# Optimization experiments

Hardware: AMD Instinct MI355X
Metric: run time of the kernel (lower is better)

Reference implementation:

```python
import jax, jax.numpy as jnp
import numpy as np

D_MODEL = 512
HEAD = 64

def setup_inputs() -> dict:
    key = jax.random.key(0)
    ks = jax.random.split(key, 7)
    s_in = 1.0 / np.sqrt(D_MODEL)
    x = jax.random.normal(ks[0], (4, 4096, D_MODEL), dtype=jnp.float32)
    Wk = jax.random.uniform(ks[1], (D_MODEL, HEAD), jnp.float32, -s_in, s_in)
    bk = jax.random.uniform(ks[2], (HEAD,), jnp.float32, -s_in, s_in)
    Wq = jax.random.uniform(ks[3], (D_MODEL, HEAD), jnp.float32, -s_in, s_in)
    bq = jax.random.uniform(ks[4], (HEAD,), jnp.float32, -s_in, s_in)
    Wv = jax.random.uniform(ks[5], (D_MODEL, HEAD), jnp.float32, -s_in, s_in)
    bv = jax.random.uniform(ks[6], (HEAD,), jnp.float32, -s_in, s_in)
    return {"x": x, "Wk": Wk, "bk": bk, "Wq": Wq, "bq": bq, "Wv": Wv, "bv": bv}

def reference(x, Wk, bk, Wq, bq, Wv, bv):
    B, T, C = x.shape
    k = x @ Wk + bk            # [B,T,H]
    q = x @ Wq + bq            # [B,T,H]
    v = x @ Wv + bv            # [B,T,H]
    scale = C ** (-0.5)
    # NOTE: original computes k @ q^T (keys index rows), softmax over query axis
    w = jnp.einsum('bkh,bqh->bkq', k, q) * scale  # [B,T,T]
    w = jax.nn.softmax(w, axis=-1)
    out = jnp.einsum('bkq,bqh->bkh', w, v)        # [B,T,H]
    return out
```

## Files before the change

### kernel.cpp

```cpp
#include <hip/hip_runtime.h>


#define DM 512
#define HD 64
#define TSEQ 4096
#define KSCALE (1.4426950408889634f * 0.04419417382415922f)

typedef __attribute__((ext_vector_type(8))) __bf16 bf16x8;
typedef __attribute__((ext_vector_type(4))) __bf16 bf16x4;
typedef __attribute__((ext_vector_type(2))) __bf16 bf16x2;
typedef __attribute__((ext_vector_type(4))) float f32x4;
typedef __attribute__((ext_vector_type(16))) float f32x16;
typedef __attribute__((ext_vector_type(4))) unsigned int uint4v;

__device__ __forceinline__ float fast_exp2(float x) {
#if __has_builtin(__builtin_amdgcn_exp2f)
    return __builtin_amdgcn_exp2f(x);
#else
    return exp2f(x);
#endif
}

__device__ __forceinline__ bf16x8 ld_bf16x8(const unsigned short* p) {
    return __builtin_bit_cast(bf16x8, *(const uint4v*)p);
}
__device__ __forceinline__ f32x4 mfma16(bf16x8 a, bf16x8 b, f32x4 c) {
    return __builtin_amdgcn_mfma_f32_16x16x32_bf16(a, b, c, 0, 0, 0);
}
__device__ __forceinline__ f32x16 mfma32(bf16x8 a, bf16x8 b, f32x16 c) {
    return __builtin_amdgcn_mfma_f32_32x32x16_bf16(a, b, c, 0, 0, 0);
}

typedef const __attribute__((address_space(1))) unsigned int* gas_t;
typedef __attribute__((address_space(3))) unsigned int* las_t;
__device__ __forceinline__ void async_cp16(const void* g, void* l) {
    __builtin_amdgcn_global_load_lds((gas_t)(unsigned long long)g,
                                     (las_t)(unsigned int)(unsigned long long)l,
                                     16, 0, 0);
}

__global__ __launch_bounds__(256) void prep_wt(const float* __restrict__ Wk,
                                               const float* __restrict__ Wq,
                                               const float* __restrict__ Wv,
                                               unsigned short* __restrict__ WT) {
    int e = blockIdx.x * 256 + threadIdx.x;
    int m = e >> 15;
    int idx = e & 32767;
    int h = idx >> 9;
    int cc = idx & 511;
    const float* W = (m == 0) ? Wk : ((m == 1) ? Wq : Wv);
    float v = W[cc * HD + h];
    if (m == 0) v *= KSCALE;
    ((__bf16*)WT)[m * 32768 + h * DM + cc] = (__bf16)v;
}

__global__ __launch_bounds__(256, 4) void proj(const float* __restrict__ x,
                                               const unsigned short* __restrict__ WT,
                                               const float* __restrict__ bk,
                                               const float* __restrict__ bq,
                                               const float* __restrict__ bv,
                                               unsigned short* __restrict__ Kw,
                                               unsigned short* __restrict__ Qw,
                                               unsigned short* __restrict__ VTw) {
    __shared__ alignas(16) float xs[8192];
    const int tid = threadIdx.x;
    const int wv = tid >> 6, lane = tid & 63;
    const int c = lane & 15, quad = lane >> 4;
    const int bx = blockIdx.x;
    const int n0 = wv * 16;

#pragma unroll
    for (int r = 0; r < 8; ++r) {
        int cid = r * 256 + tid;
        int row = cid >> 7, pos = cid & 127;
        int g = (pos & ~7) | ((pos ^ row) & 7);
        async_cp16((const char*)x + (size_t)(bx * 16 + row) * 2048 + g * 16,
                   (char*)xs + r * 4096 + wv * 1024);
    }
    __builtin_amdgcn_s_waitcnt(0x0f70);
    __syncthreads();

    const unsigned short* wtb = WT + (n0 + c) * DM + quad * 8;
    f32x4 acc[3];
#pragma unroll
    for (int m = 0; m < 3; ++m) acc[m] = (f32x4){0.f, 0.f, 0.f, 0.f};

#pragma unroll
    for (int ks = 0; ks < 16; ++ks) {
        int p0 = ks * 8 + quad * 2;
        int sp0 = (p0 & ~7) | ((p0 ^ c) & 7);
        int sp1 = ((p0 + 1) & ~7) | (((p0 + 1) ^ c) & 7);
        f32x4 xa = *(const f32x4*)((const char*)xs + c * 2048 + sp0 * 16);
        f32x4 xb = *(const f32x4*)((const char*)xs + c * 2048 + sp1 * 16);
        bf16x8 af;
        af[0] = (__bf16)xa[0]; af[1] = (__bf16)xa[1]; af[2] = (__bf16)xa[2]; af[3] = (__bf16)xa[3];
        af[4] = (__bf16)xb[0]; af[5] = (__bf16)xb[1]; af[6] = (__bf16)xb[2]; af[7] = (__bf16)xb[3];
#pragma unroll
        for (int m = 0; m < 3; ++m) {
            bf16x8 bf = ld_bf16x8(wtb + m * 32768 + ks * 32);
            acc[m] = mfma16(af, bf, acc[m]);
        }
    }

    const int row0 = bx * 16 + quad * 4;
#pragma unroll
    for (int m = 0; m < 3; ++m) {
        const float* bp = (m == 0) ? bk : ((m == 1) ? bq : bv);
        float bias = bp[n0 + c];
        if (m == 0) bias *= KSCALE;
        if (m < 2) {
            __bf16* dst = (__bf16*)((m == 0) ? Kw : Qw);
#pragma unroll
            for (int r = 0; r < 4; ++r)
                dst[(row0 + r) * HD + n0 + c] = (__bf16)(acc[m][r] + bias);
        } else {
            bf16x4 pk;
#pragma unroll
            for (int r = 0; r < 4; ++r) pk[r] = (__bf16)(acc[m][r] + bias);
            int b = bx >> 8;
            int t16 = bx & 255;
            int pj = t16 >> 1;
            int jsub = (t16 & 1) * 16 + quad * 4;
            *(bf16x4*)(VTw + (((size_t)(b * 128 + pj)) * 64 + n0 + c) * 32 + jsub) = pk;
        }
    }
}

__global__ __launch_bounds__(512, 2) void attn(const unsigned short* __restrict__ Kw,
                                               const unsigned short* __restrict__ Qw,
                                               const unsigned short* __restrict__ VTw,
                                               float* __restrict__ Op,
                                               float* __restrict__ Lp) {
    __shared__ alignas(16) char smem[36864];

    const int tid = threadIdx.x;
    const int wv = tid >> 6, lane = tid & 63;
    const int l5 = lane >> 5, l31 = lane & 31;
    const int rg = wv >> 2, jc = wv & 3;
    const int bx = blockIdx.x;
    const int batch = bx >> 6, js = (bx >> 5) & 1, tile = bx & 31;
    const int rowbase = batch * TSEQ + tile * 128;

    bf16x8 kf[2][4];
#pragma unroll
    for (int it = 0; it < 2; ++it) {
        const unsigned short* kp = Kw + (size_t)(rowbase + rg * 64 + it * 32 + l31) * HD;
#pragma unroll
        for (int ks = 0; ks < 4; ++ks) kf[it][ks] = ld_bf16x8(kp + ks * 16 + l5 * 8);
    }

    const char* qg = (const char*)Qw
                   + ((size_t)(batch * TSEQ + js * 2048 + jc * 32 + l31)) * 128
                   + l5 * 16;
    const char* vg = (const char*)VTw
                   + ((size_t)(batch * 128 + js * 64 + jc)) * 4096
                   + l31 * 64 + l5 * 16;

    f32x16 o00, o01, o10, o11;
#pragma unroll
    for (int r = 0; r < 16; ++r) { o00[r] = 0.f; o01[r] = 0.f; o10[r] = 0.f; o11[r] = 0.f; }
    float lac0 = 0.f, lac1 = 0.f;

    bf16x8 qa[4], vf[2][2];
#pragma unroll
    for (int ks = 0; ks < 4; ++ks) qa[ks] = ld_bf16x8((const unsigned short*)(qg + ks * 32));
#pragma unroll
    for (int ht = 0; ht < 2; ++ht)
#pragma unroll
        for (int k2 = 0; k2 < 2; ++k2)
            vf[ht][k2] = ld_bf16x8((const unsigned short*)(vg + ht * 2048 + k2 * 32));

    for (int jt = 0; jt < 16; ++jt) {
        bf16x8 qn[4], vn[2][2];
        if (jt < 15) {
            const char* q1 = qg + (size_t)(jt + 1) * 16384;
            const char* v1 = vg + (size_t)(jt + 1) * 16384;
#pragma unroll
            for (int ks = 0; ks < 4; ++ks) qn[ks] = ld_bf16x8((const unsigned short*)(q1 + ks * 32));
#pragma unroll
            for (int ht = 0; ht < 2; ++ht)
#pragma unroll
                for (int k2 = 0; k2 < 2; ++k2)
                    vn[ht][k2] = ld_bf16x8((const unsigned short*)(v1 + ht * 2048 + k2 * 32));
        }

        f32x16 s0, s1;
#pragma unroll
        for (int r = 0; r < 16; ++r) { s0[r] = 0.f; s1[r] = 0.f; }
#pragma unroll
        for (int ks = 0; ks < 4; ++ks) {
            s0 = mfma32(qa[ks], kf[0][ks], s0);
            s1 = mfma32(qa[ks], kf[1][ks], s1);
        }

        unsigned int pk0[8], pk1[8];
#pragma unroll
        for (int m = 0; m < 8; ++m) {
            float a0 = fast_exp2(s0[2 * m]), a1 = fast_exp2(s0[2 * m + 1]);
            float b0 = fast_exp2(s1[2 * m]), b1 = fast_exp2(s1[2 * m + 1]);
            lac0 += a0 + a1;
            lac1 += b0 + b1;
            bf16x2 ta; ta[0] = (__bf16)a0; ta[1] = (__bf16)a1;
            bf16x2 tb; tb[0] = (__bf16)b0; tb[1] = (__bf16)b1;
            pk0[m] = __builtin_bit_cast(unsigned int, ta);
            pk1[m] = __builtin_bit_cast(unsigned int, tb);
        }

#pragma unroll
        for (int k2 = 0; k2 < 2; ++k2) {
            bf16x8 pb0, pb1;
            {
                unsigned int A0 = pk0[k2 * 4 + 0], A1 = pk0[k2 * 4 + 1];
                unsigned int B0 = pk0[k2 * 4 + 2], B1 = pk0[k2 * 4 + 3];
                unsigned int t0 = l5 ? A0 : B0, t1 = l5 ? A1 : B1;
                unsigned int r0 = (unsigned int)__shfl_xor((int)t0, 32, 64);
                unsigned int r1 = (unsigned int)__shfl_xor((int)t1, 32, 64);
                uint4v u;
                u[0] = l5 ? r0 : A0; u[1] = l5 ? r1 : A1;
                u[2] = l5 ? B0 : r0; u[3] = l5 ? B1 : r1;
                pb0 = __builtin_bit_cast(bf16x8, u);
            }
            {
                unsigned int A0 = pk1[k2 * 4 + 0], A1 = pk1[k2 * 4 + 1];
                unsigned int B0 = pk1[k2 * 4 + 2], B1 = pk1[k2 * 4 + 3];
                unsigned int t0 = l5 ? A0 : B0, t1 = l5 ? A1 : B1;
                unsigned int r0 = (unsigned int)__shfl_xor((int)t0, 32, 64);
                unsigned int r1 = (unsigned int)__shfl_xor((int)t1, 32, 64);
                uint4v u;
                u[0] = l5 ? r0 : A0; u[1] = l5 ? r1 : A1;
                u[2] = l5 ? B0 : r0; u[3] = l5 ? B1 : r1;
                pb1 = __builtin_bit_cast(bf16x8, u);
            }
            o00 = mfma32(vf[0][k2], pb0, o00);
            o01 = mfma32(vf[0][k2], pb1, o01);
            o10 = mfma32(vf[1][k2], pb0, o10);
            o11 = mfma32(vf[1][k2], pb1, o11);
        }

#pragma unroll
        for (int ks = 0; ks < 4; ++ks) qa[ks] = qn[ks];
#pragma unroll
        for (int ht = 0; ht < 2; ++ht)
#pragma unroll
            for (int k2 = 0; k2 < 2; ++k2) vf[ht][k2] = vn[ht][k2];
    }

    lac0 += __shfl_xor(lac0, 32, 64);
    lac1 += __shfl_xor(lac1, 32, 64);
    __syncthreads();
    float* OCp = (float*)smem;
    float* ldsl = (float*)(smem + 34816);
    if (l5 == 0) {
        ldsl[jc * 128 + rg * 64 + l31] = lac0;
        ldsl[jc * 128 + rg * 64 + 32 + l31] = lac1;
    }

#pragma unroll
    for (int ph = 0; ph < 4; ++ph) {
        const int ht = ph >> 1, ih = ph & 1;
        __syncthreads();
        if (rg == ih) {
            const f32x16 oa = ht ? o10 : o00;
            const f32x16 ob = ht ? o11 : o01;
#pragma unroll
            for (int r = 0; r < 16; ++r) {
                int hr = (r & 3) + 8 * (r >> 2) + 4 * l5;
                OCp[(jc * 32 + hr) * 68 + l31] = oa[r];
                OCp[(jc * 32 + hr) * 68 + 32 + l31] = ob[r];
            }
        }
        __syncthreads();
#pragma unroll
        for (int rep = 0; rep < 4; ++rep) {
            int idx = rep * 512 + tid;
            int i = idx >> 5, hr = idx & 31;
            float v = OCp[(0 * 32 + hr) * 68 + i] + OCp[(1 * 32 + hr) * 68 + i]
                    + OCp[(2 * 32 + hr) * 68 + i] + OCp[(3 * 32 + hr) * 68 + i];
            Op[(size_t)js * 1048576 + (size_t)(rowbase + ih * 64 + i) * HD + ht * 32 + hr] = v;
        }
        if (ph == 0 && tid < 128) {
            float L = ldsl[tid] + ldsl[128 + tid] + ldsl[256 + tid] + ldsl[384 + tid];
            Lp[js * 16384 + rowbase + tid] = L;
        }
    }
}

__global__ __launch_bounds__(512) void fin(const float* __restrict__ Op,
                                           const float* __restrict__ Lp,
                                           float* __restrict__ out) {
    int idx = blockIdx.x * 512 + threadIdx.x;
    int e = idx * 4;
    int row = e >> 6;
    f32x4 a = *(const f32x4*)(Op + e);
    f32x4 b = *(const f32x4*)(Op + 1048576 + e);
    float L = Lp[row] + Lp[16384 + row];
    f32x4 r;
#pragma unroll
    for (int k = 0; k < 4; ++k) r[k] = (a[k] + b[k]) / L;
    *(f32x4*)(out + e) = r;
}

extern "C" void kernel_launch(void* const* d_in, const int* in_sizes, int n_in,
                              void* d_out, int out_size, void* d_ws, size_t ws_size,
                              hipStream_t stream) {
    (void)in_sizes; (void)n_in; (void)out_size; (void)ws_size;
    const float* x  = (const float*)d_in[0];
    const float* Wk = (const float*)d_in[1];
    const float* bk = (const float*)d_in[2];
    const float* Wq = (const float*)d_in[3];
    const float* bq = (const float*)d_in[4];
    const float* Wv = (const float*)d_in[5];
    const float* bv = (const float*)d_in[6];

    char* ws = (char*)d_ws;
    unsigned short* WT  = (unsigned short*)(ws);
    unsigned short* Kw  = (unsigned short*)(ws + 196608);
    unsigned short* Qw  = (unsigned short*)(ws + 2293760);
    unsigned short* VTw = (unsigned short*)(ws + 4390912);
    float* Opart        = (float*)(ws + 6488064);
    float* Lpart        = (float*)(ws + 14876672);
    float* outp = (float*)d_out;

    hipLaunchKernelGGL(prep_wt, dim3(384), dim3(256), 0, stream, Wk, Wq, Wv, WT);
    hipLaunchKernelGGL(proj, dim3(1024), dim3(256), 0, stream,
                       x, WT, bk, bq, bv, Kw, Qw, VTw);
    hipLaunchKernelGGL(attn, dim3(256), dim3(512), 0, stream, Kw, Qw, VTw, Opart, Lpart);
    hipLaunchKernelGGL(fin, dim3(512), dim3(512), 0, stream, Opart, Lpart, outp);
}
```

Measured before the change: 141.3 us.

## Stage Q/V tiles in swizzled LDS via async copies and split keys four ways

The attention kernel now uses 256-thread blocks over 64 key rows with four query-range splits, giving 1024 blocks instead of 256. Per iteration, shared Q and V^T tiles are loaded into XOR-swizzled LDS with async 16-byte copies, so all waves reuse them instead of each wave fetching its own fragments into registers from global memory. The finishing kernel now sums four partial outputs and four normalisers. This trades the register-level prefetch pipelining for block barriers and LDS traffic. It also doubles the partial-output workspace and the final reduction's reads.

```diff
diff --git a/kernel.cpp b/kernel.cpp
--- a/kernel.cpp
+++ b/kernel.cpp
@@ -126,7 +126,7 @@
     }
 }
 
-__global__ __launch_bounds__(512, 2) void attn(const unsigned short* __restrict__ Kw,
+__global__ __launch_bounds__(256, 3) void attn(const unsigned short* __restrict__ Kw,
                                                const unsigned short* __restrict__ Qw,
                                                const unsigned short* __restrict__ VTw,
                                                float* __restrict__ Op,
@@ -136,61 +136,64 @@
     const int tid = threadIdx.x;
     const int wv = tid >> 6, lane = tid & 63;
     const int l5 = lane >> 5, l31 = lane & 31;
-    const int rg = wv >> 2, jc = wv & 3;
+    const int jw = wv;
     const int bx = blockIdx.x;
-    const int batch = bx >> 6, js = (bx >> 5) & 1, tile = bx & 31;
-    const int rowbase = batch * TSEQ + tile * 128;
+    const int itile = bx & 63, jq = (bx >> 6) & 3, batch = bx >> 8;
+    const int rowbase = batch * TSEQ + itile * 64;
 
     bf16x8 kf[2][4];
 #pragma unroll
     for (int it = 0; it < 2; ++it) {
-        const unsigned short* kp = Kw + (size_t)(rowbase + rg * 64 + it * 32 + l31) * HD;
+        const unsigned short* kp = Kw + (size_t)(rowbase + it * 32 + l31) * HD;
 #pragma unroll
         for (int ks = 0; ks < 4; ++ks) kf[it][ks] = ld_bf16x8(kp + ks * 16 + l5 * 8);
     }
 
-    const char* qg = (const char*)Qw
-                   + ((size_t)(batch * TSEQ + js * 2048 + jc * 32 + l31)) * 128
-                   + l5 * 16;
-    const char* vg = (const char*)VTw
-                   + ((size_t)(batch * 128 + js * 64 + jc)) * 4096
-                   + l31 * 64 + l5 * 16;
+    const int jrow = jw * 32 + l31;
+    int qoff[4];
+#pragma unroll
+    for (int ks = 0; ks < 4; ++ks)
+        qoff[ks] = jrow * 128 + (((ks * 2 + l5) ^ (jrow & 7)) * 16);
+    int voff[2][2];
+#pragma unroll
+    for (int ht = 0; ht < 2; ++ht)
+#pragma unroll
+        for (int k2 = 0; k2 < 2; ++k2)
+            voff[ht][k2] = jw * 4096 + (ht * 32 + l31) * 64 + (((k2 * 2 + l5) ^ (l31 & 3)) * 16);
+
+    const int qlo = (lane >> 3) * 128 + (((lane & 7) ^ ((lane >> 3) & 7)) * 16);
+    const int vlo = (lane >> 2) * 64 + (((lane & 3) ^ ((lane >> 2) & 3)) * 16);
+    const char* qsrc = (const char*)Qw + (size_t)(batch * TSEQ + jq * 1024) * 128;
+    const char* vsrc = (const char*)VTw + (size_t)(batch * 128 + jq * 32) * 4096;
+    char* QL = smem;
+    char* VL = smem + 16384;
 
     f32x16 o00, o01, o10, o11;
 #pragma unroll
     for (int r = 0; r < 16; ++r) { o00[r] = 0.f; o01[r] = 0.f; o10[r] = 0.f; o11[r] = 0.f; }
     float lac0 = 0.f, lac1 = 0.f;
 
-    bf16x8 qa[4], vf[2][2];
-#pragma unroll
-    for (int ks = 0; ks < 4; ++ks) qa[ks] = ld_bf16x8((const unsigned short*)(qg + ks * 32));
-#pragma unroll
-    for (int ht = 0; ht < 2; ++ht)
-#pragma unroll
-        for (int k2 = 0; k2 < 2; ++k2)
-            vf[ht][k2] = ld_bf16x8((const unsigned short*)(vg + ht * 2048 + k2 * 32));
-
-    for (int jt = 0; jt < 16; ++jt) {
-        bf16x8 qn[4], vn[2][2];
-        if (jt < 15) {
-            const char* q1 = qg + (size_t)(jt + 1) * 16384;
-            const char* v1 = vg + (size_t)(jt + 1) * 16384;
-#pragma unroll
-            for (int ks = 0; ks < 4; ++ks) qn[ks] = ld_bf16x8((const unsigned short*)(q1 + ks * 32));
-#pragma unroll
-            for (int ht = 0; ht < 2; ++ht)
-#pragma unroll
-                for (int k2 = 0; k2 < 2; ++k2)
-                    vn[ht][k2] = ld_bf16x8((const unsigned short*)(v1 + ht * 2048 + k2 * 32));
-        }
+    for (int jt = 0; jt < 8; ++jt) {
+        if (jt) __syncthreads();
+        const char* qs = qsrc + (size_t)jt * 16384;
+        const char* vs = vsrc + (size_t)jt * 16384;
+#pragma unroll
+        for (int rd = 0; rd < 8; ++rd)
+            async_cp16(qs + rd * 4096 + wv * 1024 + qlo, QL + rd * 4096 + wv * 1024);
+#pragma unroll
+        for (int rv = 0; rv < 4; ++rv)
+            async_cp16(vs + rv * 4096 + wv * 1024 + vlo, VL + rv * 4096 + wv * 1024);
+        __builtin_amdgcn_s_waitcnt(0x0f70);
+        __syncthreads();
 
         f32x16 s0, s1;
 #pragma unroll
         for (int r = 0; r < 16; ++r) { s0[r] = 0.f; s1[r] = 0.f; }
 #pragma unroll
         for (int ks = 0; ks < 4; ++ks) {
-            s0 = mfma32(qa[ks], kf[0][ks], s0);
-            s1 = mfma32(qa[ks], kf[1][ks], s1);
+            bf16x8 qa = ld_bf16x8((const unsigned short*)(QL + qoff[ks]));
+            s0 = mfma32(qa, kf[0][ks], s0);
+            s1 = mfma32(qa, kf[1][ks], s1);
         }
 
         unsigned int pk0[8], pk1[8];
@@ -231,18 +234,13 @@
                 u[2] = l5 ? B0 : r0; u[3] = l5 ? B1 : r1;
                 pb1 = __builtin_bit_cast(bf16x8, u);
             }
-            o00 = mfma32(vf[0][k2], pb0, o00);
-            o01 = mfma32(vf[0][k2], pb1, o01);
-            o10 = mfma32(vf[1][k2], pb0, o10);
-            o11 = mfma32(vf[1][k2], pb1, o11);
-        }
-
-#pragma unroll
-        for (int ks = 0; ks < 4; ++ks) qa[ks] = qn[ks];
-#pragma unroll
-        for (int ht = 0; ht < 2; ++ht)
-#pragma unroll
-            for (int k2 = 0; k2 < 2; ++k2) vf[ht][k2] = vn[ht][k2];
+            bf16x8 vf0 = ld_bf16x8((const unsigned short*)(VL + voff[0][k2]));
+            bf16x8 vf1 = ld_bf16x8((const unsigned short*)(VL + voff[1][k2]));
+            o00 = mfma32(vf0, pb0, o00);
+            o01 = mfma32(vf0, pb1, o01);
+            o10 = mfma32(vf1, pb0, o10);
+            o11 = mfma32(vf1, pb1, o11);
+        }
     }
 
     lac0 += __shfl_xor(lac0, 32, 64);
@@ -251,52 +249,53 @@
     float* OCp = (float*)smem;
     float* ldsl = (float*)(smem + 34816);
     if (l5 == 0) {
-        ldsl[jc * 128 + rg * 64 + l31] = lac0;
-        ldsl[jc * 128 + rg * 64 + 32 + l31] = lac1;
-    }
-
-#pragma unroll
-    for (int ph = 0; ph < 4; ++ph) {
-        const int ht = ph >> 1, ih = ph & 1;
+        ldsl[jw * 64 + l31] = lac0;
+        ldsl[jw * 64 + 32 + l31] = lac1;
+    }
+
+#pragma unroll
+    for (int ht = 0; ht < 2; ++ht) {
+        const f32x16 oa = ht ? o10 : o00;
+        const f32x16 ob = ht ? o11 : o01;
+#pragma unroll
+        for (int r = 0; r < 16; ++r) {
+            int hr = (r & 3) + 8 * (r >> 2) + 4 * l5;
+            OCp[(jw * 32 + hr) * 68 + l31] = oa[r];
+            OCp[(jw * 32 + hr) * 68 + 32 + l31] = ob[r];
+        }
         __syncthreads();
-        if (rg == ih) {
-            const f32x16 oa = ht ? o10 : o00;
-            const f32x16 ob = ht ? o11 : o01;
-#pragma unroll
-            for (int r = 0; r < 16; ++r) {
-                int hr = (r & 3) + 8 * (r >> 2) + 4 * l5;
-                OCp[(jc * 32 + hr) * 68 + l31] = oa[r];
-                OCp[(jc * 32 + hr) * 68 + 32 + l31] = ob[r];
-            }
-        }
-        __syncthreads();
-#pragma unroll
-        for (int rep = 0; rep < 4; ++rep) {
-            int idx = rep * 512 + tid;
+#pragma unroll
+        for (int rep = 0; rep < 8; ++rep) {
+            int idx = rep * 256 + tid;
             int i = idx >> 5, hr = idx & 31;
             float v = OCp[(0 * 32 + hr) * 68 + i] + OCp[(1 * 32 + hr) * 68 + i]
                     + OCp[(2 * 32 + hr) * 68 + i] + OCp[(3 * 32 + hr) * 68 + i];
-            Op[(size_t)js * 1048576 + (size_t)(rowbase + ih * 64 + i) * HD + ht * 32 + hr] = v;
-        }
-        if (ph == 0 && tid < 128) {
-            float L = ldsl[tid] + ldsl[128 + tid] + ldsl[256 + tid] + ldsl[384 + tid];
-            Lp[js * 16384 + rowbase + tid] = L;
-        }
-    }
-}
-
-__global__ __launch_bounds__(512) void fin(const float* __restrict__ Op,
+            Op[(size_t)jq * 1048576 + (size_t)(rowbase + i) * HD + ht * 32 + hr] = v;
+        }
+        if (ht == 0) {
+            if (tid < 64) {
+                float L = ldsl[tid] + ldsl[64 + tid] + ldsl[128 + tid] + ldsl[192 + tid];
+                Lp[jq * 16384 + rowbase + tid] = L;
+            }
+            __syncthreads();
+        }
+    }
+}
+
+__global__ __launch_bounds__(256) void fin(const float* __restrict__ Op,
                                            const float* __restrict__ Lp,
                                            float* __restrict__ out) {
-    int idx = blockIdx.x * 512 + threadIdx.x;
+    int idx = blockIdx.x * 256 + threadIdx.x;
     int e = idx * 4;
     int row = e >> 6;
     f32x4 a = *(const f32x4*)(Op + e);
     f32x4 b = *(const f32x4*)(Op + 1048576 + e);
-    float L = Lp[row] + Lp[16384 + row];
+    f32x4 c = *(const f32x4*)(Op + 2097152 + e);
+    f32x4 d = *(const f32x4*)(Op + 3145728 + e);
+    float L = Lp[row] + Lp[16384 + row] + Lp[32768 + row] + Lp[49152 + row];
     f32x4 r;
 #pragma unroll
-    for (int k = 0; k < 4; ++k) r[k] = (a[k] + b[k]) / L;
+    for (int k = 0; k < 4; ++k) r[k] = (a[k] + b[k] + c[k] + d[k]) / L;
     *(f32x4*)(out + e) = r;
 }
 
@@ -318,12 +317,12 @@
     unsigned short* Qw  = (unsigned short*)(ws + 2293760);
     unsigned short* VTw = (unsigned short*)(ws + 4390912);
     float* Opart        = (float*)(ws + 6488064);
-    float* Lpart        = (float*)(ws + 14876672);
+    float* Lpart        = (float*)(ws + 23265280);
     float* outp = (float*)d_out;
 
     hipLaunchKernelGGL(prep_wt, dim3(384), dim3(256), 0, stream, Wk, Wq, Wv, WT);
     hipLaunchKernelGGL(proj, dim3(1024), dim3(256), 0, stream,
                        x, WT, bk, bq, bv, Kw, Qw, VTw);
-    hipLaunchKernelGGL(attn, dim3(256), dim3(512), 0, stream, Kw, Qw, VTw, Opart, Lpart);
-    hipLaunchKernelGGL(fin, dim3(512), dim3(512), 0, stream, Opart, Lpart, outp);
-}
+    hipLaunchKernelGGL(attn, dim3(1024), dim3(256), 0, stream, Kw, Qw, VTw, Opart, Lpart);
+    hipLaunchKernelGGL(fin, dim3(1024), dim3(256), 0, stream, Opart, Lpart, outp);
+}
```

Measured after the change: 151.7 us. 7.4% more time.
